# Performance work log

Measured on AMD Instinct MI355X. Metric: run time of the kernel, lower is better.

## Reference

```python
import jax, jax.numpy as jnp
import numpy as np

BN_INV = 1.0 / np.sqrt(1.0 + 1e-5)  # eval-mode BatchNorm1d with running_mean=0, running_var=1


def _lin_bn_relu(x, W, g, b):
    # Linear(no bias) -> BN(eval) -> ReLU
    return jax.nn.relu((x @ W.T) * (g * BN_INV) + b)


def setup_inputs() -> dict:
    key = jax.random.key(0)
    ks = jax.random.split(key, 24)
    B, P, N, C, H, OUT = 8, 1024, 20, 32, 256, 256
    s = 0.05
    inp = {
        "polylines": jax.random.normal(ks[0], (B, P, N, C), dtype=jnp.float32),
        "polylines_mask": jax.random.randint(ks[1], (B, P, N), 0, 2) > 0,
        # pre_mlps: [Lin(C->H,no bias)+BN+ReLU] x2, Lin(H->H, bias)
        "pre_w0": jax.random.normal(ks[2], (H, C), dtype=jnp.float32) * s,
        "pre_g0": jnp.ones((H,), jnp.float32),
        "pre_b0": jnp.zeros((H,), jnp.float32),
        "pre_w1": jax.random.normal(ks[3], (H, H), dtype=jnp.float32) * s,
        "pre_g1": jnp.ones((H,), jnp.float32),
        "pre_b1": jnp.zeros((H,), jnp.float32),
        "pre_w2": jax.random.normal(ks[4], (H, H), dtype=jnp.float32) * s,
        "pre_bias2": jnp.zeros((H,), jnp.float32),
        # mlps: c_in=2H -> [H,H,H]
        "mlp_w0": jax.random.normal(ks[5], (H, 2 * H), dtype=jnp.float32) * s,
        "mlp_g0": jnp.ones((H,), jnp.float32),
        "mlp_b0": jnp.zeros((H,), jnp.float32),
        "mlp_w1": jax.random.normal(ks[6], (H, H), dtype=jnp.float32) * s,
        "mlp_g1": jnp.ones((H,), jnp.float32),
        "mlp_b1": jnp.zeros((H,), jnp.float32),
        "mlp_w2": jax.random.normal(ks[7], (H, H), dtype=jnp.float32) * s,
        "mlp_bias2": jnp.zeros((H,), jnp.float32),
        # out_mlps (without_norm): Lin(H->H,bias)+ReLU, Lin(H->OUT,bias)
        "out_w0": jax.random.normal(ks[8], (H, H), dtype=jnp.float32) * s,
        "out_b0": jnp.zeros((H,), jnp.float32),
        "out_w1": jax.random.normal(ks[9], (OUT, H), dtype=jnp.float32) * s,
        "out_b1": jnp.zeros((OUT,), jnp.float32),
    }
    return inp


def reference(polylines, polylines_mask,
              pre_w0, pre_g0, pre_b0, pre_w1, pre_g1, pre_b1, pre_w2, pre_bias2,
              mlp_w0, mlp_g0, mlp_b0, mlp_w1, mlp_g1, mlp_b1, mlp_w2, mlp_bias2,
              out_w0, out_b0, out_w1, out_b1):
    # gather->MLP->zero-scatter is equivalent to dense MLP followed by mask-zeroing
    # (all per-point ops are elementwise / last-dim matmuls).
    m = polylines_mask[..., None].astype(polylines.dtype)  # (B,P,N,1)

    x = _lin_bn_relu(polylines, pre_w0, pre_g0, pre_b0)
    x = _lin_bn_relu(x, pre_w1, pre_g1, pre_b1)
    x = (x @ pre_w2.T + pre_bias2) * m                      # (B,P,N,H) zero at invalid

    pooled = x.max(axis=2)                                  # (B,P,H) max over zero-filled buffer
    x = jnp.concatenate(
        [x, jnp.broadcast_to(pooled[:, :, None, :], x.shape)], axis=-1)  # (B,P,N,2H)

    x = _lin_bn_relu(x, mlp_w0, mlp_g0, mlp_b0)
    x = _lin_bn_relu(x, mlp_w1, mlp_g1, mlp_b1)
    x = (x @ mlp_w2.T + mlp_bias2) * m                      # (B,P,N,H)

    buf = x.max(axis=2)                                     # (B,P,H)

    valid = jnp.any(polylines_mask, axis=-1)                # sum(mask)>0
    y = jax.nn.relu(buf @ out_w0.T + out_b0)
    y = (y @ out_w1.T + out_b1) * valid[..., None].astype(buf.dtype)  # (B,P,OUT)
    return y
```

## Files before the change

kernel.cpp:

```cpp
#include <hip/hip_runtime.h>
#include <stdint.h>
#include <stddef.h>

typedef __bf16 bf16;
typedef __bf16 bf16x4 __attribute__((ext_vector_type(4)));
typedef __bf16 bf16x8 __attribute__((ext_vector_type(8)));
typedef float f32x4 __attribute__((ext_vector_type(4)));
typedef float f32x16 __attribute__((ext_vector_type(16)));

#define BNI 0.9999950000374996f
#define NROW 240
#define NPOLYB 12
#define TOTROW 163840
#define NPOLY 8192
#define NBLK 683

#define AADDR(r, ch) ((r)*256 + ((((ch) ^ ((r)&31)))<<3))

#define OFF_ACT  0
#define OFF_WB0  122880
#define OFF_WB1  139264
#define OFF_T2   155648
#define OFF_VAL  161792
#define LDS_TOTAL 161840

#define WS_PRE_W0 0
#define WS_PRE_W1 8192
#define WS_PRE_W2 73728
#define WS_MLP_W0 139264
#define WS_MLP_W1 270336
#define WS_MLP_W2 335872
#define WS_OUT_W0 401408
#define WS_OUT_W1 466944

__device__ __forceinline__ bf16 f2b(float f){
  unsigned int i = __builtin_bit_cast(unsigned int, f);
  unsigned int r = i + 0x7fffu + ((i >> 16) & 1u);
  unsigned short h = (unsigned short)(r >> 16);
  return __builtin_bit_cast(bf16, h);
}
__device__ __forceinline__ float b2f(bf16 x){
  unsigned short u = __builtin_bit_cast(unsigned short, x);
  union { unsigned int i; float f; } v; v.i = ((unsigned int)u) << 16; return v.f;
}
__device__ __forceinline__ bf16x8 ld8f(const float* p, float sc){
  f32x4 a = *(const f32x4*)p;
  f32x4 b = *(const f32x4*)(p + 4);
  bf16x8 r;
  #pragma unroll
  for (int j = 0; j < 4; ++j){ r[j] = f2b(a[j]*sc); r[4+j] = f2b(b[j]*sc); }
  return r;
}

__global__ __launch_bounds__(256)
void prep_kernel(const float* s0, const float* s1, const float* s2, const float* s3,
                 const float* s4, const float* s5, const float* s6, const float* s7,
                 const float* g0, const float* g1, const float* g3, const float* g4,
                 bf16* dst)
{
  const int offs[8] = {WS_PRE_W0, WS_PRE_W1, WS_PRE_W2, WS_MLP_W0,
                       WS_MLP_W1, WS_MLP_W2, WS_OUT_W0, WS_OUT_W1};
  const int sz[8]   = {8192, 65536, 65536, 131072, 65536, 65536, 65536, 65536};
  const int ld[8]   = {32, 256, 256, 512, 256, 256, 256, 256};
  int r = blockIdx.y;
  const float* src = s0;
  if (r == 1) src = s1; else if (r == 2) src = s2; else if (r == 3) src = s3;
  else if (r == 4) src = s4; else if (r == 5) src = s5; else if (r == 6) src = s6;
  else if (r == 7) src = s7;
  const float* gp = (r==0)?g0:(r==1)?g1:(r==3)?g3:(r==4)?g4:nullptr;
  int i = (blockIdx.x*256 + threadIdx.x)*8;
  if (i < sz[r]){
    float sc = gp ? gp[i/ld[r]]*BNI : 1.0f;
    *(bf16x8*)&dst[offs[r] + i] = ld8f(src + i, sc);
  }
}

__device__ __forceinline__ void stageAsync32(const bf16* W, int ldK, int nt, bf16* buf, int tid){
  int wv = tid >> 6;
  #pragma unroll
  for (int i = 0; i < 2; ++i){
    int id = tid + 512*i;
    int fr = id >> 5, kcd = id & 31;
    int kcs = kcd ^ (fr & 31);
    const bf16* g = W + (size_t)(nt*32 + fr)*ldK + kcs*8;
    bf16* l = buf + (size_t)(wv*64 + 512*i)*8;
    __builtin_amdgcn_global_load_lds(
        (const __attribute__((address_space(1))) void*)g,
        (__attribute__((address_space(3))) void*)l,
        16, 0, 0);
  }
}

template<int RELU, int MASK, int ADDT2>
__device__ __forceinline__ void epiT(
    const f32x16& acc, int nt, int row, int poly, float mk, bool valid,
    bf16* sAct, const bf16* sT2, const float* bptr, int hi)
{
  #pragma unroll
  for (int q2 = 0; q2 < 4; ++q2){
    int f0 = nt*32 + 8*q2 + 4*hi;
    f32x4 bb = *(const f32x4*)(bptr + f0);
    bf16x4 tv = {};
    if (ADDT2) tv = *(const bf16x4*)&sT2[poly*256 + f0];
    bf16x4 o;
    #pragma unroll
    for (int j = 0; j < 4; ++j){
      float v = acc[4*q2 + j];
      if (ADDT2) v += b2f(tv[j]);
      v += bb[j];
      if (RELU) v = fmaxf(v, 0.0f);
      if (MASK) v *= mk;
      o[j] = f2b(v);
    }
    if (valid)
      *(bf16x4*)&sAct[row*256 + (((nt*4 + q2) ^ (row & 31))<<3) + 4*hi] = o;
  }
}

template<int RELU, int MASK, int ADDT2>
__device__ __forceinline__ void layerT(
    bf16* sAct, bf16* wb0, bf16* wb1, const bf16* sT2,
    const bf16* W, int ldK, const float* bptr,
    const int* maskp, int blk, int row, int rowc, int lane32, int hi, int tid)
{
  bf16x8 B[16];
  #pragma unroll
  for (int t = 0; t < 16; ++t)
    B[t] = *(const bf16x8*)&sAct[AADDR(rowc, 2*t + hi)];

  float mk = 1.0f;
  if (MASK){
    int g = blk*NROW + row;
    mk = (row < NROW && g < TOTROW && maskp[g]) ? 1.0f : 0.0f;
  }
  const int poly = rowc/20;
  const bool valid = row < NROW;

  stageAsync32(W, ldK, 0, wb0, tid);
  __syncthreads();
  #pragma unroll 1
  for (int c = 0; c < 8; ++c){
    const bf16* cur = (c & 1) ? wb1 : wb0;
    bf16* nxt = (c & 1) ? wb0 : wb1;
    if (c < 7) stageAsync32(W, ldK, c + 1, nxt, tid);
    bf16x8 wf[16];
    const bf16* base = cur + lane32*256;
    #pragma unroll
    for (int t = 0; t < 16; ++t)
      wf[t] = *(const bf16x8*)(base + (((2*t + hi) ^ (lane32 & 31))<<3));
    f32x16 acc = {};
    #pragma unroll
    for (int t = 0; t < 16; ++t)
      acc = __builtin_amdgcn_mfma_f32_32x32x16_bf16(wf[t], B[t], acc, 0, 0, 0);
    epiT<RELU,MASK,ADDT2>(acc, c, row, poly, mk, valid, sAct, sT2, bptr, hi);
    __syncthreads();
  }
}

__device__ __forceinline__ void poolT(const bf16* sAct, bf16* sPool, int tid){
  if (tid < 384){
    int poly = tid >> 5, c = tid & 31;
    float m[8];
    bf16x8 v0 = *(const bf16x8*)&sAct[AADDR(poly*20, c)];
    #pragma unroll
    for (int j = 0; j < 8; ++j) m[j] = b2f(v0[j]);
    for (int r = 1; r < 20; ++r){
      bf16x8 v = *(const bf16x8*)&sAct[AADDR(poly*20 + r, c)];
      #pragma unroll
      for (int j = 0; j < 8; ++j) m[j] = fmaxf(m[j], b2f(v[j]));
    }
    bf16x8 o;
    #pragma unroll
    for (int j = 0; j < 8; ++j) o[j] = f2b(m[j]);
    *(bf16x8*)&sPool[AADDR(poly, c)] = o;
  }
}

__global__ __launch_bounds__(512) __attribute__((amdgpu_waves_per_eu(2, 2)))
void traj_kernel(const float* __restrict__ poly, const int* __restrict__ maskp,
                 const float* pre_b0, const float* pre_b1, const float* pre_bias2,
                 const float* mlp_b0, const float* mlp_b1, const float* mlp_bias2,
                 const float* out_b0, const float* out_b1,
                 const bf16* __restrict__ ws,
                 float* __restrict__ outp)
{
  extern __shared__ char smem[];
  bf16*  sAct   = (bf16*)(smem + OFF_ACT);
  bf16*  wb0    = (bf16*)(smem + OFF_WB0);
  bf16*  wb1    = (bf16*)(smem + OFF_WB1);
  bf16*  sT2    = (bf16*)(smem + OFF_T2);
  float* sValid = (float*)(smem + OFF_VAL);
  bf16*  sPool  = wb0;
  bf16*  sY     = sAct;

  const int tid = threadIdx.x;
  const int w = tid >> 6, L = tid & 63, lane32 = L & 31, hi = L >> 5;
  const int row  = w*32 + lane32;
  const int rowc = row < NROW ? row : NROW - 1;
  const int blk = blockIdx.x;

  const bf16* pw0 = ws + WS_PRE_W0;
  const bf16* pw1 = ws + WS_PRE_W1;
  const bf16* pw2 = ws + WS_PRE_W2;
  const bf16* mw0 = ws + WS_MLP_W0;
  const bf16* mw1 = ws + WS_MLP_W1;
  const bf16* mw2 = ws + WS_MLP_W2;
  const bf16* ow0 = ws + WS_OUT_W0;
  const bf16* ow1 = ws + WS_OUT_W1;

  #pragma unroll
  for (int i = 0; i < 2; ++i){
    int id = tid + 512*i;
    if (id < 960){
      int r = id >> 2, c = id & 3;
      int grow = blk*NROW + r;
      bf16x8 v = {};
      if (grow < TOTROW) v = ld8f(poly + (size_t)grow*32 + c*8, 1.0f);
      *(bf16x8*)&sAct[AADDR(r, c)] = v;
    }
  }
  __syncthreads();
  if (tid < NPOLYB){
    float v = 0.0f;
    #pragma unroll
    for (int r = 0; r < 20; ++r){
      int g = blk*NROW + tid*20 + r;
      if (g < TOTROW && maskp[g]) v = 1.0f;
    }
    sValid[tid] = v;
  }

  {
    bf16x8 B0 = *(const bf16x8*)&sAct[AADDR(rowc, hi)];
    bf16x8 B1 = *(const bf16x8*)&sAct[AADDR(rowc, 2 + hi)];
    #pragma unroll 1
    for (int nt = 0; nt < 8; ++nt){
      const bf16* p = pw0 + (size_t)(nt*32 + lane32)*32 + 8*hi;
      bf16x8 w0 = *(const bf16x8*)p;
      bf16x8 w1 = *(const bf16x8*)(p + 16);
      f32x16 acc = {};
      acc = __builtin_amdgcn_mfma_f32_32x32x16_bf16(w0, B0, acc, 0, 0, 0);
      acc = __builtin_amdgcn_mfma_f32_32x32x16_bf16(w1, B1, acc, 0, 0, 0);
      epiT<1,0,0>(acc, nt, row, 0, 1.0f, row < NROW, sAct, sT2, pre_b0, hi);
    }
  }
  __syncthreads();

  layerT<1,0,0>(sAct, wb0, wb1, sT2, pw1, 256, pre_b1,    maskp, blk, row, rowc, lane32, hi, tid);
  layerT<0,1,0>(sAct, wb0, wb1, sT2, pw2, 256, pre_bias2, maskp, blk, row, rowc, lane32, hi, tid);

  poolT(sAct, sPool, tid);
  __syncthreads();

  {
    bf16x8 Bp[16];
    #pragma unroll
    for (int t = 0; t < 16; ++t)
      Bp[t] = *(const bf16x8*)&sPool[AADDR((lane32 < NPOLYB ? lane32 : 0), 2*t + hi)];
    int nt = w;
    const bf16* p = mw0 + (size_t)(nt*32 + lane32)*512 + 256 + 8*hi;
    f32x16 acc = {};
    #pragma unroll
    for (int t = 0; t < 16; ++t){
      bf16x8 wf = *(const bf16x8*)(p + 16*t);
      acc = __builtin_amdgcn_mfma_f32_32x32x16_bf16(wf, Bp[t], acc, 0, 0, 0);
    }
    if (lane32 < NPOLYB){
      #pragma unroll
      for (int q2 = 0; q2 < 4; ++q2){
        int f0 = nt*32 + 8*q2 + 4*hi;
        bf16x4 o;
        #pragma unroll
        for (int j = 0; j < 4; ++j) o[j] = f2b(acc[4*q2 + j]);
        *(bf16x4*)&sT2[lane32*256 + f0] = o;
      }
    }
  }
  __syncthreads();

  layerT<1,0,1>(sAct, wb0, wb1, sT2, mw0, 512, mlp_b0,    maskp, blk, row, rowc, lane32, hi, tid);
  layerT<1,0,0>(sAct, wb0, wb1, sT2, mw1, 256, mlp_b1,    maskp, blk, row, rowc, lane32, hi, tid);
  layerT<0,1,0>(sAct, wb0, wb1, sT2, mw2, 256, mlp_bias2, maskp, blk, row, rowc, lane32, hi, tid);

  poolT(sAct, sPool, tid);
  __syncthreads();

  {
    bf16x8 Bp[16];
    #pragma unroll
    for (int t = 0; t < 16; ++t)
      Bp[t] = *(const bf16x8*)&sPool[AADDR((lane32 < NPOLYB ? lane32 : 0), 2*t + hi)];
    int nt = w;
    const bf16* p = ow0 + (size_t)(nt*32 + lane32)*256 + 8*hi;
    f32x16 acc = {};
    #pragma unroll
    for (int t = 0; t < 16; ++t){
      bf16x8 wf = *(const bf16x8*)(p + 16*t);
      acc = __builtin_amdgcn_mfma_f32_32x32x16_bf16(wf, Bp[t], acc, 0, 0, 0);
    }
    if (lane32 < NPOLYB){
      #pragma unroll
      for (int q2 = 0; q2 < 4; ++q2){
        int f0 = nt*32 + 8*q2 + 4*hi;
        f32x4 bb = *(const f32x4*)(out_b0 + f0);
        bf16x4 o;
        #pragma unroll
        for (int j = 0; j < 4; ++j) o[j] = f2b(fmaxf(acc[4*q2 + j] + bb[j], 0.0f));
        *(bf16x4*)&sY[lane32*256 + (((nt*4 + q2) ^ (lane32 & 31))<<3) + 4*hi] = o;
      }
    }
  }
  __syncthreads();

  {
    bf16x8 By[16];
    #pragma unroll
    for (int t = 0; t < 16; ++t)
      By[t] = *(const bf16x8*)&sY[AADDR((lane32 < NPOLYB ? lane32 : 0), 2*t + hi)];
    int gp = blk*NPOLYB + lane32;
    float vd = (lane32 < NPOLYB) ? sValid[lane32] : 0.0f;
    int nt = w;
    const bf16* p = ow1 + (size_t)(nt*32 + lane32)*256 + 8*hi;
    f32x16 acc = {};
    #pragma unroll
    for (int t = 0; t < 16; ++t){
      bf16x8 wf = *(const bf16x8*)(p + 16*t);
      acc = __builtin_amdgcn_mfma_f32_32x32x16_bf16(wf, By[t], acc, 0, 0, 0);
    }
    if (lane32 < NPOLYB && gp < NPOLY){
      #pragma unroll
      for (int q2 = 0; q2 < 4; ++q2){
        int f0 = nt*32 + 8*q2 + 4*hi;
        f32x4 bb = *(const f32x4*)(out_b1 + f0);
        f32x4 o;
        #pragma unroll
        for (int j = 0; j < 4; ++j) o[j] = (acc[4*q2 + j] + bb[j]) * vd;
        *(f32x4*)&outp[(size_t)gp*256 + f0] = o;
      }
    }
  }
}

extern "C" void kernel_launch(void* const* d_in, const int* in_sizes, int n_in,
                              void* d_out, int out_size, void* d_ws, size_t ws_size,
                              hipStream_t stream)
{
  const float* poly      = (const float*)d_in[0];
  const int*   maskp     = (const int*)  d_in[1];
  const float* pre_w0    = (const float*)d_in[2];
  const float* pre_g0    = (const float*)d_in[3];
  const float* pre_b0    = (const float*)d_in[4];
  const float* pre_w1    = (const float*)d_in[5];
  const float* pre_g1    = (const float*)d_in[6];
  const float* pre_b1    = (const float*)d_in[7];
  const float* pre_w2    = (const float*)d_in[8];
  const float* pre_bias2 = (const float*)d_in[9];
  const float* mlp_w0    = (const float*)d_in[10];
  const float* mlp_g0    = (const float*)d_in[11];
  const float* mlp_b0    = (const float*)d_in[12];
  const float* mlp_w1    = (const float*)d_in[13];
  const float* mlp_g1    = (const float*)d_in[14];
  const float* mlp_b1    = (const float*)d_in[15];
  const float* mlp_w2    = (const float*)d_in[16];
  const float* mlp_bias2 = (const float*)d_in[17];
  const float* out_w0    = (const float*)d_in[18];
  const float* out_b0    = (const float*)d_in[19];
  const float* out_w1    = (const float*)d_in[20];
  const float* out_b1    = (const float*)d_in[21];

  bf16* ws = (bf16*)d_ws;

  (void)hipFuncSetAttribute((const void*)&traj_kernel,
                            hipFuncAttributeMaxDynamicSharedMemorySize, LDS_TOTAL);

  prep_kernel<<<dim3(64, 8), dim3(256), 0, stream>>>(
      pre_w0, pre_w1, pre_w2, mlp_w0, mlp_w1, mlp_w2, out_w0, out_w1,
      pre_g0, pre_g1, mlp_g0, mlp_g1, ws);

  traj_kernel<<<dim3(NBLK), dim3(512), LDS_TOTAL, stream>>>(
      poly, maskp,
      pre_b0, pre_b1, pre_bias2,
      mlp_b0, mlp_b1, mlp_bias2,
      out_b0, out_b1,
      ws, (float*)d_out);
}
```

Baseline: 303.9 us.

## Double block to 1024 threads, splitting output tiles across two wave groups

Measured after the change: 326.0 us. +7.3%, slower.

```diff
diff --git a/kernel.cpp b/kernel.cpp
--- a/kernel.cpp
+++ b/kernel.cpp
@@ -19,7 +19,6 @@
 
 #define OFF_ACT  0
 #define OFF_WB0  122880
-#define OFF_WB1  139264
 #define OFF_T2   155648
 #define OFF_VAL  161792
 #define LDS_TOTAL 161840
@@ -75,20 +74,17 @@
   }
 }
 
-__device__ __forceinline__ void stageAsync32(const bf16* W, int ldK, int nt, bf16* buf, int tid){
-  int wv = tid >> 6;
-  #pragma unroll
-  for (int i = 0; i < 2; ++i){
-    int id = tid + 512*i;
-    int fr = id >> 5, kcd = id & 31;
-    int kcs = kcd ^ (fr & 31);
-    const bf16* g = W + (size_t)(nt*32 + fr)*ldK + kcs*8;
-    bf16* l = buf + (size_t)(wv*64 + 512*i)*8;
-    __builtin_amdgcn_global_load_lds(
-        (const __attribute__((address_space(1))) void*)g,
-        (__attribute__((address_space(3))) void*)l,
-        16, 0, 0);
-  }
+__device__ __forceinline__ void stageAsyncG(const bf16* W, int ldK, int tile, int kh,
+                                            bf16* buf, int wg, int lane){
+  int id = wg*64 + lane;
+  int fr = id >> 4, kcd = id & 15;
+  int kcs = kcd ^ (fr & 15);
+  const bf16* gp = W + (size_t)(tile*32 + fr)*ldK + kh*128 + kcs*8;
+  bf16* l = buf + (size_t)(wg*64)*8;
+  __builtin_amdgcn_global_load_lds(
+      (const __attribute__((address_space(1))) void*)gp,
+      (__attribute__((address_space(3))) void*)l,
+      16, 0, 0);
 }
 
 template<int RELU, int MASK, int ADDT2>
@@ -118,10 +114,11 @@
 }
 
 template<int RELU, int MASK, int ADDT2>
-__device__ __forceinline__ void layerT(
-    bf16* sAct, bf16* wb0, bf16* wb1, const bf16* sT2,
+__device__ __forceinline__ void layerT16(
+    bf16* sAct, bf16* wbase, const bf16* sT2,
     const bf16* W, int ldK, const float* bptr,
-    const int* maskp, int blk, int row, int rowc, int lane32, int hi, int tid)
+    const int* maskp, int blk, int g, int wg, int row, int rowc,
+    int lane32, int hi, int lane)
 {
   bf16x8 B[16];
   #pragma unroll
@@ -130,29 +127,45 @@
 
   float mk = 1.0f;
   if (MASK){
-    int g = blk*NROW + row;
-    mk = (row < NROW && g < TOTROW && maskp[g]) ? 1.0f : 0.0f;
+    int gr = blk*NROW + row;
+    mk = (row < NROW && gr < TOTROW && maskp[gr]) ? 1.0f : 0.0f;
   }
   const int poly = rowc/20;
   const bool valid = row < NROW;
-
-  stageAsync32(W, ldK, 0, wb0, tid);
+  bf16* bufA = wbase + (size_t)(2*g)*4096;
+  bf16* bufB = bufA + 4096;
+
+  stageAsyncG(W, ldK, g*4, 0, bufA, wg, lane);
   __syncthreads();
   #pragma unroll 1
-  for (int c = 0; c < 8; ++c){
-    const bf16* cur = (c & 1) ? wb1 : wb0;
-    bf16* nxt = (c & 1) ? wb0 : wb1;
-    if (c < 7) stageAsync32(W, ldK, c + 1, nxt, tid);
-    bf16x8 wf[16];
-    const bf16* base = cur + lane32*256;
-    #pragma unroll
-    for (int t = 0; t < 16; ++t)
-      wf[t] = *(const bf16x8*)(base + (((2*t + hi) ^ (lane32 & 31))<<3));
-    f32x16 acc = {};
-    #pragma unroll
-    for (int t = 0; t < 16; ++t)
-      acc = __builtin_amdgcn_mfma_f32_32x32x16_bf16(wf[t], B[t], acc, 0, 0, 0);
-    epiT<RELU,MASK,ADDT2>(acc, c, row, poly, mk, valid, sAct, sT2, bptr, hi);
+  for (int p = 0; p < 4; ++p){
+    f32x16 acc;
+    stageAsyncG(W, ldK, g*4 + p, 1, bufB, wg, lane);
+    {
+      bf16x8 wf[8];
+      const bf16* base = bufA + lane32*128;
+      #pragma unroll
+      for (int t = 0; t < 8; ++t)
+        wf[t] = *(const bf16x8*)(base + (((2*t + hi) ^ (lane32 & 15))<<3));
+      #pragma unroll
+      for (int j = 0; j < 16; ++j) acc[j] = 0.0f;
+      #pragma unroll
+      for (int t = 0; t < 8; ++t)
+        acc = __builtin_amdgcn_mfma_f32_32x32x16_bf16(wf[t], B[t], acc, 0, 0, 0);
+    }
+    __syncthreads();
+    if (p < 3) stageAsyncG(W, ldK, g*4 + p + 1, 0, bufA, wg, lane);
+    {
+      bf16x8 wf[8];
+      const bf16* base = bufB + lane32*128;
+      #pragma unroll
+      for (int t = 0; t < 8; ++t)
+        wf[t] = *(const bf16x8*)(base + (((2*t + hi) ^ (lane32 & 15))<<3));
+      #pragma unroll
+      for (int t = 0; t < 8; ++t)
+        acc = __builtin_amdgcn_mfma_f32_32x32x16_bf16(wf[t], B[8 + t], acc, 0, 0, 0);
+      epiT<RELU,MASK,ADDT2>(acc, g*4 + p, row, poly, mk, valid, sAct, sT2, bptr, hi);
+    }
     __syncthreads();
   }
 }
@@ -176,7 +189,7 @@
   }
 }
 
-__global__ __launch_bounds__(512) __attribute__((amdgpu_waves_per_eu(2, 2)))
+__global__ __launch_bounds__(1024) __attribute__((amdgpu_waves_per_eu(4, 4)))
 void traj_kernel(const float* __restrict__ poly, const int* __restrict__ maskp,
                  const float* pre_b0, const float* pre_b1, const float* pre_bias2,
                  const float* mlp_b0, const float* mlp_b1, const float* mlp_bias2,
@@ -186,16 +199,16 @@
 {
   extern __shared__ char smem[];
   bf16*  sAct   = (bf16*)(smem + OFF_ACT);
-  bf16*  wb0    = (bf16*)(smem + OFF_WB0);
-  bf16*  wb1    = (bf16*)(smem + OFF_WB1);
+  bf16*  wbase  = (bf16*)(smem + OFF_WB0);
   bf16*  sT2    = (bf16*)(smem + OFF_T2);
   float* sValid = (float*)(smem + OFF_VAL);
-  bf16*  sPool  = wb0;
+  bf16*  sPool  = wbase;
   bf16*  sY     = sAct;
 
   const int tid = threadIdx.x;
   const int w = tid >> 6, L = tid & 63, lane32 = L & 31, hi = L >> 5;
-  const int row  = w*32 + lane32;
+  const int g = w >> 3, wg = w & 7;
+  const int row  = wg*32 + lane32;
   const int rowc = row < NROW ? row : NROW - 1;
   const int blk = blockIdx.x;
 
@@ -208,24 +221,20 @@
   const bf16* ow0 = ws + WS_OUT_W0;
   const bf16* ow1 = ws + WS_OUT_W1;
 
-  #pragma unroll
-  for (int i = 0; i < 2; ++i){
-    int id = tid + 512*i;
-    if (id < 960){
-      int r = id >> 2, c = id & 3;
-      int grow = blk*NROW + r;
-      bf16x8 v = {};
-      if (grow < TOTROW) v = ld8f(poly + (size_t)grow*32 + c*8, 1.0f);
-      *(bf16x8*)&sAct[AADDR(r, c)] = v;
-    }
+  if (tid < 960){
+    int r = tid >> 2, c = tid & 3;
+    int grow = blk*NROW + r;
+    bf16x8 v = {};
+    if (grow < TOTROW) v = ld8f(poly + (size_t)grow*32 + c*8, 1.0f);
+    *(bf16x8*)&sAct[AADDR(r, c)] = v;
   }
   __syncthreads();
   if (tid < NPOLYB){
     float v = 0.0f;
     #pragma unroll
     for (int r = 0; r < 20; ++r){
-      int g = blk*NROW + tid*20 + r;
-      if (g < TOTROW && maskp[g]) v = 1.0f;
+      int gg = blk*NROW + tid*20 + r;
+      if (gg < TOTROW && maskp[gg]) v = 1.0f;
     }
     sValid[tid] = v;
   }
@@ -233,8 +242,10 @@
   {
     bf16x8 B0 = *(const bf16x8*)&sAct[AADDR(rowc, hi)];
     bf16x8 B1 = *(const bf16x8*)&sAct[AADDR(rowc, 2 + hi)];
+    __syncthreads();
     #pragma unroll 1
-    for (int nt = 0; nt < 8; ++nt){
+    for (int ntl = 0; ntl < 4; ++ntl){
+      int nt = g*4 + ntl;
       const bf16* p = pw0 + (size_t)(nt*32 + lane32)*32 + 8*hi;
       bf16x8 w0 = *(const bf16x8*)p;
       bf16x8 w1 = *(const bf16x8*)(p + 16);
@@ -246,13 +257,13 @@
   }
   __syncthreads();
 
-  layerT<1,0,0>(sAct, wb0, wb1, sT2, pw1, 256, pre_b1,    maskp, blk, row, rowc, lane32, hi, tid);
-  layerT<0,1,0>(sAct, wb0, wb1, sT2, pw2, 256, pre_bias2, maskp, blk, row, rowc, lane32, hi, tid);
+  layerT16<1,0,0>(sAct, wbase, sT2, pw1, 256, pre_b1,    maskp, blk, g, wg, row, rowc, lane32, hi, L);
+  layerT16<0,1,0>(sAct, wbase, sT2, pw2, 256, pre_bias2, maskp, blk, g, wg, row, rowc, lane32, hi, L);
 
   poolT(sAct, sPool, tid);
   __syncthreads();
 
-  {
+  if (w < 8){
     bf16x8 Bp[16];
     #pragma unroll
     for (int t = 0; t < 16; ++t)
@@ -278,14 +289,14 @@
   }
   __syncthreads();
 
-  layerT<1,0,1>(sAct, wb0, wb1, sT2, mw0, 512, mlp_b0,    maskp, blk, row, rowc, lane32, hi, tid);
-  layerT<1,0,0>(sAct, wb0, wb1, sT2, mw1, 256, mlp_b1,    maskp, blk, row, rowc, lane32, hi, tid);
-  layerT<0,1,0>(sAct, wb0, wb1, sT2, mw2, 256, mlp_bias2, maskp, blk, row, rowc, lane32, hi, tid);
+  layerT16<1,0,1>(sAct, wbase, sT2, mw0, 512, mlp_b0,    maskp, blk, g, wg, row, rowc, lane32, hi, L);
+  layerT16<1,0,0>(sAct, wbase, sT2, mw1, 256, mlp_b1,    maskp, blk, g, wg, row, rowc, lane32, hi, L);
+  layerT16<0,1,0>(sAct, wbase, sT2, mw2, 256, mlp_bias2, maskp, blk, g, wg, row, rowc, lane32, hi, L);
 
   poolT(sAct, sPool, tid);
   __syncthreads();
 
-  {
+  if (w < 8){
     bf16x8 Bp[16];
     #pragma unroll
     for (int t = 0; t < 16; ++t)
@@ -312,7 +323,7 @@
   }
   __syncthreads();
 
-  {
+  if (w < 8){
     bf16x8 By[16];
     #pragma unroll
     for (int t = 0; t < 16; ++t)
@@ -377,7 +388,7 @@
       pre_w0, pre_w1, pre_w2, mlp_w0, mlp_w1, mlp_w2, out_w0, out_w1,
       pre_g0, pre_g1, mlp_g0, mlp_g1, ws);
 
-  traj_kernel<<<dim3(NBLK), dim3(512), LDS_TOTAL, stream>>>(
+  traj_kernel<<<dim3(NBLK), dim3(1024), LDS_TOTAL, stream>>>(
       poly, maskp,
       pre_b0, pre_b1, pre_bias2,
       mlp_b0, mlp_b1, mlp_bias2,
```

## Halve block to 4 waves, each wave computing two row tiles per weight fragment

Applied to the files above, without the earlier changes.

After: 371.1 us. 1.22x slower.

```diff
diff --git a/kernel.cpp b/kernel.cpp
--- a/kernel.cpp
+++ b/kernel.cpp
@@ -78,12 +78,12 @@
 __device__ __forceinline__ void stageAsync32(const bf16* W, int ldK, int nt, bf16* buf, int tid){
   int wv = tid >> 6;
   #pragma unroll
-  for (int i = 0; i < 2; ++i){
-    int id = tid + 512*i;
+  for (int i = 0; i < 4; ++i){
+    int id = tid + 256*i;
     int fr = id >> 5, kcd = id & 31;
     int kcs = kcd ^ (fr & 31);
     const bf16* g = W + (size_t)(nt*32 + fr)*ldK + kcs*8;
-    bf16* l = buf + (size_t)(wv*64 + 512*i)*8;
+    bf16* l = buf + (size_t)(wv*64 + 256*i)*8;
     __builtin_amdgcn_global_load_lds(
         (const __attribute__((address_space(1))) void*)g,
         (__attribute__((address_space(3))) void*)l,
@@ -118,23 +118,53 @@
 }
 
 template<int RELU, int MASK, int ADDT2>
-__device__ __forceinline__ void layerT(
+__device__ __forceinline__ void epiTb(
+    const f32x16& acc, int nt, int row, int poly, float mk, bool valid,
+    bf16* sAct, const bf16* sT2, int hi,
+    const f32x4& bbA, const f32x4& bbB, const f32x4& bbC, const f32x4& bbD)
+{
+  #pragma unroll
+  for (int q2 = 0; q2 < 4; ++q2){
+    int f0 = nt*32 + 8*q2 + 4*hi;
+    f32x4 bb = (q2==0) ? bbA : (q2==1) ? bbB : (q2==2) ? bbC : bbD;
+    bf16x4 tv = {};
+    if (ADDT2) tv = *(const bf16x4*)&sT2[poly*256 + f0];
+    bf16x4 o;
+    #pragma unroll
+    for (int j = 0; j < 4; ++j){
+      float v = acc[4*q2 + j];
+      if (ADDT2) v += b2f(tv[j]);
+      v += bb[j];
+      if (RELU) v = fmaxf(v, 0.0f);
+      if (MASK) v *= mk;
+      o[j] = f2b(v);
+    }
+    if (valid)
+      *(bf16x4*)&sAct[row*256 + (((nt*4 + q2) ^ (row & 31))<<3) + 4*hi] = o;
+  }
+}
+
+template<int RELU, int MASK, int ADDT2>
+__device__ __forceinline__ void layerW4(
     bf16* sAct, bf16* wb0, bf16* wb1, const bf16* sT2,
     const bf16* W, int ldK, const float* bptr,
-    const int* maskp, int blk, int row, int rowc, int lane32, int hi, int tid)
-{
-  bf16x8 B[16];
-  #pragma unroll
-  for (int t = 0; t < 16; ++t)
-    B[t] = *(const bf16x8*)&sAct[AADDR(rowc, 2*t + hi)];
-
-  float mk = 1.0f;
+    const int* maskp, int blk, int row0, int row1,
+    int rowc0, int rowc1, int lane32, int hi, int tid)
+{
+  bf16x8 B0[16], B1[16];
+  #pragma unroll
+  for (int t = 0; t < 16; ++t){
+    B0[t] = *(const bf16x8*)&sAct[AADDR(rowc0, 2*t + hi)];
+    B1[t] = *(const bf16x8*)&sAct[AADDR(rowc1, 2*t + hi)];
+  }
+  float mk0 = 1.0f, mk1 = 1.0f;
   if (MASK){
-    int g = blk*NROW + row;
-    mk = (row < NROW && g < TOTROW && maskp[g]) ? 1.0f : 0.0f;
-  }
-  const int poly = rowc/20;
-  const bool valid = row < NROW;
+    int g0 = blk*NROW + row0, g1 = blk*NROW + row1;
+    mk0 = (row0 < NROW && g0 < TOTROW && maskp[g0]) ? 1.0f : 0.0f;
+    mk1 = (row1 < NROW && g1 < TOTROW && maskp[g1]) ? 1.0f : 0.0f;
+  }
+  const int poly0 = rowc0/20, poly1 = rowc1/20;
+  const bool valid0 = row0 < NROW, valid1 = row1 < NROW;
 
   stageAsync32(W, ldK, 0, wb0, tid);
   __syncthreads();
@@ -143,23 +173,28 @@
     const bf16* cur = (c & 1) ? wb1 : wb0;
     bf16* nxt = (c & 1) ? wb0 : wb1;
     if (c < 7) stageAsync32(W, ldK, c + 1, nxt, tid);
-    bf16x8 wf[16];
+    const float* bp = bptr + c*32 + 4*hi;
+    f32x4 bbA = *(const f32x4*)(bp);
+    f32x4 bbB = *(const f32x4*)(bp + 8);
+    f32x4 bbC = *(const f32x4*)(bp + 16);
+    f32x4 bbD = *(const f32x4*)(bp + 24);
+    f32x16 acc0 = {}, acc1 = {};
     const bf16* base = cur + lane32*256;
     #pragma unroll
-    for (int t = 0; t < 16; ++t)
-      wf[t] = *(const bf16x8*)(base + (((2*t + hi) ^ (lane32 & 31))<<3));
-    f32x16 acc = {};
-    #pragma unroll
-    for (int t = 0; t < 16; ++t)
-      acc = __builtin_amdgcn_mfma_f32_32x32x16_bf16(wf[t], B[t], acc, 0, 0, 0);
-    epiT<RELU,MASK,ADDT2>(acc, c, row, poly, mk, valid, sAct, sT2, bptr, hi);
+    for (int t = 0; t < 16; ++t){
+      bf16x8 wf = *(const bf16x8*)(base + (((2*t + hi) ^ (lane32 & 31))<<3));
+      acc0 = __builtin_amdgcn_mfma_f32_32x32x16_bf16(wf, B0[t], acc0, 0, 0, 0);
+      acc1 = __builtin_amdgcn_mfma_f32_32x32x16_bf16(wf, B1[t], acc1, 0, 0, 0);
+    }
+    epiTb<RELU,MASK,ADDT2>(acc0, c, row0, poly0, mk0, valid0, sAct, sT2, hi, bbA, bbB, bbC, bbD);
+    epiTb<RELU,MASK,ADDT2>(acc1, c, row1, poly1, mk1, valid1, sAct, sT2, hi, bbA, bbB, bbC, bbD);
     __syncthreads();
   }
 }
 
 __device__ __forceinline__ void poolT(const bf16* sAct, bf16* sPool, int tid){
-  if (tid < 384){
-    int poly = tid >> 5, c = tid & 31;
+  for (int u = tid; u < 384; u += 256){
+    int poly = u >> 5, c = u & 31;
     float m[8];
     bf16x8 v0 = *(const bf16x8*)&sAct[AADDR(poly*20, c)];
     #pragma unroll
@@ -176,7 +211,7 @@
   }
 }
 
-__global__ __launch_bounds__(512) __attribute__((amdgpu_waves_per_eu(2, 2)))
+__global__ __launch_bounds__(256) __attribute__((amdgpu_waves_per_eu(1, 1)))
 void traj_kernel(const float* __restrict__ poly, const int* __restrict__ maskp,
                  const float* pre_b0, const float* pre_b1, const float* pre_bias2,
                  const float* mlp_b0, const float* mlp_b1, const float* mlp_bias2,
@@ -195,8 +230,10 @@
 
   const int tid = threadIdx.x;
   const int w = tid >> 6, L = tid & 63, lane32 = L & 31, hi = L >> 5;
-  const int row  = w*32 + lane32;
-  const int rowc = row < NROW ? row : NROW - 1;
+  const int row0 = w*64 + lane32;
+  const int row1 = row0 + 32;
+  const int rowc0 = row0 < NROW ? row0 : NROW - 1;
+  const int rowc1 = row1 < NROW ? row1 : NROW - 1;
   const int blk = blockIdx.x;
 
   const bf16* pw0 = ws + WS_PRE_W0;
@@ -209,8 +246,8 @@
   const bf16* ow1 = ws + WS_OUT_W1;
 
   #pragma unroll
-  for (int i = 0; i < 2; ++i){
-    int id = tid + 512*i;
+  for (int i = 0; i < 4; ++i){
+    int id = tid + 256*i;
     if (id < 960){
       int r = id >> 2, c = id & 3;
       int grow = blk*NROW + r;
@@ -231,23 +268,28 @@
   }
 
   {
-    bf16x8 B0 = *(const bf16x8*)&sAct[AADDR(rowc, hi)];
-    bf16x8 B1 = *(const bf16x8*)&sAct[AADDR(rowc, 2 + hi)];
+    bf16x8 B00 = *(const bf16x8*)&sAct[AADDR(rowc0, hi)];
+    bf16x8 B01 = *(const bf16x8*)&sAct[AADDR(rowc0, 2 + hi)];
+    bf16x8 B10 = *(const bf16x8*)&sAct[AADDR(rowc1, hi)];
+    bf16x8 B11 = *(const bf16x8*)&sAct[AADDR(rowc1, 2 + hi)];
     #pragma unroll 1
     for (int nt = 0; nt < 8; ++nt){
       const bf16* p = pw0 + (size_t)(nt*32 + lane32)*32 + 8*hi;
       bf16x8 w0 = *(const bf16x8*)p;
       bf16x8 w1 = *(const bf16x8*)(p + 16);
-      f32x16 acc = {};
-      acc = __builtin_amdgcn_mfma_f32_32x32x16_bf16(w0, B0, acc, 0, 0, 0);
-      acc = __builtin_amdgcn_mfma_f32_32x32x16_bf16(w1, B1, acc, 0, 0, 0);
-      epiT<1,0,0>(acc, nt, row, 0, 1.0f, row < NROW, sAct, sT2, pre_b0, hi);
-    }
-  }
-  __syncthreads();
-
-  layerT<1,0,0>(sAct, wb0, wb1, sT2, pw1, 256, pre_b1,    maskp, blk, row, rowc, lane32, hi, tid);
-  layerT<0,1,0>(sAct, wb0, wb1, sT2, pw2, 256, pre_bias2, maskp, blk, row, rowc, lane32, hi, tid);
+      f32x16 acc0 = {}, acc1 = {};
+      acc0 = __builtin_amdgcn_mfma_f32_32x32x16_bf16(w0, B00, acc0, 0, 0, 0);
+      acc0 = __builtin_amdgcn_mfma_f32_32x32x16_bf16(w1, B01, acc0, 0, 0, 0);
+      acc1 = __builtin_amdgcn_mfma_f32_32x32x16_bf16(w0, B10, acc1, 0, 0, 0);
+      acc1 = __builtin_amdgcn_mfma_f32_32x32x16_bf16(w1, B11, acc1, 0, 0, 0);
+      epiT<1,0,0>(acc0, nt, row0, 0, 1.0f, row0 < NROW, sAct, sT2, pre_b0, hi);
+      epiT<1,0,0>(acc1, nt, row1, 0, 1.0f, row1 < NROW, sAct, sT2, pre_b0, hi);
+    }
+  }
+  __syncthreads();
+
+  layerW4<1,0,0>(sAct, wb0, wb1, sT2, pw1, 256, pre_b1,    maskp, blk, row0, row1, rowc0, rowc1, lane32, hi, tid);
+  layerW4<0,1,0>(sAct, wb0, wb1, sT2, pw2, 256, pre_bias2, maskp, blk, row0, row1, rowc0, rowc1, lane32, hi, tid);
 
   poolT(sAct, sPool, tid);
   __syncthreads();
@@ -257,30 +299,33 @@
     #pragma unroll
     for (int t = 0; t < 16; ++t)
       Bp[t] = *(const bf16x8*)&sPool[AADDR((lane32 < NPOLYB ? lane32 : 0), 2*t + hi)];
-    int nt = w;
-    const bf16* p = mw0 + (size_t)(nt*32 + lane32)*512 + 256 + 8*hi;
-    f32x16 acc = {};
-    #pragma unroll
-    for (int t = 0; t < 16; ++t){
-      bf16x8 wf = *(const bf16x8*)(p + 16*t);
-      acc = __builtin_amdgcn_mfma_f32_32x32x16_bf16(wf, Bp[t], acc, 0, 0, 0);
-    }
-    if (lane32 < NPOLYB){
+    #pragma unroll 1
+    for (int it = 0; it < 2; ++it){
+      int nt = w + 4*it;
+      const bf16* p = mw0 + (size_t)(nt*32 + lane32)*512 + 256 + 8*hi;
+      f32x16 acc = {};
       #pragma unroll
-      for (int q2 = 0; q2 < 4; ++q2){
-        int f0 = nt*32 + 8*q2 + 4*hi;
-        bf16x4 o;
+      for (int t = 0; t < 16; ++t){
+        bf16x8 wf = *(const bf16x8*)(p + 16*t);
+        acc = __builtin_amdgcn_mfma_f32_32x32x16_bf16(wf, Bp[t], acc, 0, 0, 0);
+      }
+      if (lane32 < NPOLYB){
         #pragma unroll
-        for (int j = 0; j < 4; ++j) o[j] = f2b(acc[4*q2 + j]);
-        *(bf16x4*)&sT2[lane32*256 + f0] = o;
-      }
-    }
-  }
-  __syncthreads();
-
-  layerT<1,0,1>(sAct, wb0, wb1, sT2, mw0, 512, mlp_b0,    maskp, blk, row, rowc, lane32, hi, tid);
-  layerT<1,0,0>(sAct, wb0, wb1, sT2, mw1, 256, mlp_b1,    maskp, blk, row, rowc, lane32, hi, tid);
-  layerT<0,1,0>(sAct, wb0, wb1, sT2, mw2, 256, mlp_bias2, maskp, blk, row, rowc, lane32, hi, tid);
+        for (int q2 = 0; q2 < 4; ++q2){
+          int f0 = nt*32 + 8*q2 + 4*hi;
+          bf16x4 o;
+          #pragma unroll
+          for (int j = 0; j < 4; ++j) o[j] = f2b(acc[4*q2 + j]);
+          *(bf16x4*)&sT2[lane32*256 + f0] = o;
+        }
+      }
+    }
+  }
+  __syncthreads();
+
+  layerW4<1,0,1>(sAct, wb0, wb1, sT2, mw0, 512, mlp_b0,    maskp, blk, row0, row1, rowc0, rowc1, lane32, hi, tid);
+  layerW4<1,0,0>(sAct, wb0, wb1, sT2, mw1, 256, mlp_b1,    maskp, blk, row0, row1, rowc0, rowc1, lane32, hi, tid);
+  layerW4<0,1,0>(sAct, wb0, wb1, sT2, mw2, 256, mlp_bias2, maskp, blk, row0, row1, rowc0, rowc1, lane32, hi, tid);
 
   poolT(sAct, sPool, tid);
   __syncthreads();
@@ -290,23 +335,26 @@
     #pragma unroll
     for (int t = 0; t < 16; ++t)
       Bp[t] = *(const bf16x8*)&sPool[AADDR((lane32 < NPOLYB ? lane32 : 0), 2*t + hi)];
-    int nt = w;
-    const bf16* p = ow0 + (size_t)(nt*32 + lane32)*256 + 8*hi;
-    f32x16 acc = {};
-    #pragma unroll
-    for (int t = 0; t < 16; ++t){
-      bf16x8 wf = *(const bf16x8*)(p + 16*t);
-      acc = __builtin_amdgcn_mfma_f32_32x32x16_bf16(wf, Bp[t], acc, 0, 0, 0);
-    }
-    if (lane32 < NPOLYB){
+    #pragma unroll 1
+    for (int it = 0; it < 2; ++it){
+      int nt = w + 4*it;
+      const bf16* p = ow0 + (size_t)(nt*32 + lane32)*256 + 8*hi;
+      f32x16 acc = {};
       #pragma unroll
-      for (int q2 = 0; q2 < 4; ++q2){
-        int f0 = nt*32 + 8*q2 + 4*hi;
-        f32x4 bb = *(const f32x4*)(out_b0 + f0);
-        bf16x4 o;
+      for (int t = 0; t < 16; ++t){
+        bf16x8 wf = *(const bf16x8*)(p + 16*t);
+        acc = __builtin_amdgcn_mfma_f32_32x32x16_bf16(wf, Bp[t], acc, 0, 0, 0);
+      }
+      if (lane32 < NPOLYB){
         #pragma unroll
-        for (int j = 0; j < 4; ++j) o[j] = f2b(fmaxf(acc[4*q2 + j] + bb[j], 0.0f));
-        *(bf16x4*)&sY[lane32*256 + (((nt*4 + q2) ^ (lane32 & 31))<<3) + 4*hi] = o;
+        for (int q2 = 0; q2 < 4; ++q2){
+          int f0 = nt*32 + 8*q2 + 4*hi;
+          f32x4 bb = *(const f32x4*)(out_b0 + f0);
+          bf16x4 o;
+          #pragma unroll
+          for (int j = 0; j < 4; ++j) o[j] = f2b(fmaxf(acc[4*q2 + j] + bb[j], 0.0f));
+          *(bf16x4*)&sY[lane32*256 + (((nt*4 + q2) ^ (lane32 & 31))<<3) + 4*hi] = o;
+        }
       }
     }
   }
@@ -319,23 +367,26 @@
       By[t] = *(const bf16x8*)&sY[AADDR((lane32 < NPOLYB ? lane32 : 0), 2*t + hi)];
     int gp = blk*NPOLYB + lane32;
     float vd = (lane32 < NPOLYB) ? sValid[lane32] : 0.0f;
-    int nt = w;
-    const bf16* p = ow1 + (size_t)(nt*32 + lane32)*256 + 8*hi;
-    f32x16 acc = {};
-    #pragma unroll
-    for (int t = 0; t < 16; ++t){
-      bf16x8 wf = *(const bf16x8*)(p + 16*t);
-      acc = __builtin_amdgcn_mfma_f32_32x32x16_bf16(wf, By[t], acc, 0, 0, 0);
-    }
-    if (lane32 < NPOLYB && gp < NPOLY){
+    #pragma unroll 1
+    for (int it = 0; it < 2; ++it){
+      int nt = w + 4*it;
+      const bf16* p = ow1 + (size_t)(nt*32 + lane32)*256 + 8*hi;
+      f32x16 acc = {};
       #pragma unroll
-      for (int q2 = 0; q2 < 4; ++q2){
-        int f0 = nt*32 + 8*q2 + 4*hi;
-        f32x4 bb = *(const f32x4*)(out_b1 + f0);
-        f32x4 o;
+      for (int t = 0; t < 16; ++t){
+        bf16x8 wf = *(const bf16x8*)(p + 16*t);
+        acc = __builtin_amdgcn_mfma_f32_32x32x16_bf16(wf, By[t], acc, 0, 0, 0);
+      }
+      if (lane32 < NPOLYB && gp < NPOLY){
         #pragma unroll
-        for (int j = 0; j < 4; ++j) o[j] = (acc[4*q2 + j] + bb[j]) * vd;
-        *(f32x4*)&outp[(size_t)gp*256 + f0] = o;
+        for (int q2 = 0; q2 < 4; ++q2){
+          int f0 = nt*32 + 8*q2 + 4*hi;
+          f32x4 bb = *(const f32x4*)(out_b1 + f0);
+          f32x4 o;
+          #pragma unroll
+          for (int j = 0; j < 4; ++j) o[j] = (acc[4*q2 + j] + bb[j]) * vd;
+          *(f32x4*)&outp[(size_t)gp*256 + f0] = o;
+        }
       }
     }
   }
@@ -377,7 +428,7 @@
       pre_w0, pre_w1, pre_w2, mlp_w0, mlp_w1, mlp_w2, out_w0, out_w1,
       pre_g0, pre_g1, mlp_g0, mlp_g1, ws);
 
-  traj_kernel<<<dim3(NBLK), dim3(512), LDS_TOTAL, stream>>>(
+  traj_kernel<<<dim3(NBLK), dim3(256), LDS_TOTAL, stream>>>(
       poly, maskp,
       pre_b0, pre_b1, pre_bias2,
       mlp_b0, mlp_b1, mlp_bias2,
```

## Pre-swizzle weights into MFMA fragment order and read them directly from global

Applied to the files above, without the earlier changes.

Measured after the change: 355.5 us. 17.0% more time.

```diff
diff --git a/kernel.cpp b/kernel.cpp
--- a/kernel.cpp
+++ b/kernel.cpp
@@ -18,16 +18,16 @@
 #define AADDR(r, ch) ((r)*256 + ((((ch) ^ ((r)&31)))<<3))
 
 #define OFF_ACT  0
-#define OFF_WB0  122880
-#define OFF_WB1  139264
-#define OFF_T2   155648
-#define OFF_VAL  161792
-#define LDS_TOTAL 161840
+#define OFF_POOL 122880
+#define OFF_T2   129024
+#define OFF_VAL  135168
+#define LDS_TOTAL 135216
 
 #define WS_PRE_W0 0
 #define WS_PRE_W1 8192
 #define WS_PRE_W2 73728
 #define WS_MLP_W0 139264
+#define WS_MLP_W0T (139264 + 65536)
 #define WS_MLP_W1 270336
 #define WS_MLP_W2 335872
 #define WS_OUT_W0 401408
@@ -68,26 +68,19 @@
   else if (r == 4) src = s4; else if (r == 5) src = s5; else if (r == 6) src = s6;
   else if (r == 7) src = s7;
   const float* gp = (r==0)?g0:(r==1)?g1:(r==3)?g3:(r==4)?g4:nullptr;
-  int i = (blockIdx.x*256 + threadIdx.x)*8;
-  if (i < sz[r]){
-    float sc = gp ? gp[i/ld[r]]*BNI : 1.0f;
-    *(bf16x8*)&dst[offs[r] + i] = ld8f(src + i, sc);
-  }
-}
-
-__device__ __forceinline__ void stageAsync32(const bf16* W, int ldK, int nt, bf16* buf, int tid){
-  int wv = tid >> 6;
-  #pragma unroll
-  for (int i = 0; i < 2; ++i){
-    int id = tid + 512*i;
-    int fr = id >> 5, kcd = id & 31;
-    int kcs = kcd ^ (fr & 31);
-    const bf16* g = W + (size_t)(nt*32 + fr)*ldK + kcs*8;
-    bf16* l = buf + (size_t)(wv*64 + 512*i)*8;
-    __builtin_amdgcn_global_load_lds(
-        (const __attribute__((address_space(1))) void*)g,
-        (__attribute__((address_space(3))) void*)l,
-        16, 0, 0);
+  int gid = blockIdx.x*256 + threadIdx.x;
+  int ldv = ld[r];
+  if (gid < (sz[r] >> 3)){
+    int l, t, nt, colbase = 0;
+    if (ldv == 512){ colbase = (gid >> 13)*256; int g2 = gid & 8191;
+                     l = g2 & 63; t = (g2 >> 6) & 15; nt = g2 >> 10; }
+    else if (ldv == 256){ l = gid & 63; t = (gid >> 6) & 15; nt = gid >> 10; }
+    else { l = gid & 63; t = (gid >> 6) & 1; nt = gid >> 7; }
+    int srow = nt*32 + (l & 31);
+    int scol = colbase + t*16 + (l >> 5)*8;
+    float sc = gp ? gp[srow]*BNI : 1.0f;
+    *(bf16x8*)&dst[offs[r] + (size_t)gid*8] =
+        ld8f(src + (size_t)srow*ldv + scol, sc);
   }
 }
 
@@ -118,10 +111,9 @@
 }
 
 template<int RELU, int MASK, int ADDT2>
-__device__ __forceinline__ void layerT(
-    bf16* sAct, bf16* wb0, bf16* wb1, const bf16* sT2,
-    const bf16* W, int ldK, const float* bptr,
-    const int* maskp, int blk, int row, int rowc, int lane32, int hi, int tid)
+__device__ __forceinline__ void layerG(
+    bf16* sAct, const bf16* sT2, const bf16* __restrict__ Wf, const float* bptr,
+    const int* maskp, int blk, int row, int rowc, int hi, int L)
 {
   bf16x8 B[16];
   #pragma unroll
@@ -136,24 +128,16 @@
   const int poly = rowc/20;
   const bool valid = row < NROW;
 
-  stageAsync32(W, ldK, 0, wb0, tid);
-  __syncthreads();
   #pragma unroll 1
-  for (int c = 0; c < 8; ++c){
-    const bf16* cur = (c & 1) ? wb1 : wb0;
-    bf16* nxt = (c & 1) ? wb0 : wb1;
-    if (c < 7) stageAsync32(W, ldK, c + 1, nxt, tid);
-    bf16x8 wf[16];
-    const bf16* base = cur + lane32*256;
-    #pragma unroll
-    for (int t = 0; t < 16; ++t)
-      wf[t] = *(const bf16x8*)(base + (((2*t + hi) ^ (lane32 & 31))<<3));
+  for (int nt = 0; nt < 8; ++nt){
+    const bf16* p = Wf + (size_t)nt*8192 + (size_t)L*8;
     f32x16 acc = {};
     #pragma unroll
-    for (int t = 0; t < 16; ++t)
-      acc = __builtin_amdgcn_mfma_f32_32x32x16_bf16(wf[t], B[t], acc, 0, 0, 0);
-    epiT<RELU,MASK,ADDT2>(acc, c, row, poly, mk, valid, sAct, sT2, bptr, hi);
-    __syncthreads();
+    for (int t = 0; t < 16; ++t){
+      bf16x8 wf = *(const bf16x8*)(p + t*512);
+      acc = __builtin_amdgcn_mfma_f32_32x32x16_bf16(wf, B[t], acc, 0, 0, 0);
+    }
+    epiT<RELU,MASK,ADDT2>(acc, nt, row, poly, mk, valid, sAct, sT2, bptr, hi);
   }
 }
 
@@ -186,11 +170,9 @@
 {
   extern __shared__ char smem[];
   bf16*  sAct   = (bf16*)(smem + OFF_ACT);
-  bf16*  wb0    = (bf16*)(smem + OFF_WB0);
-  bf16*  wb1    = (bf16*)(smem + OFF_WB1);
+  bf16*  sPool  = (bf16*)(smem + OFF_POOL);
   bf16*  sT2    = (bf16*)(smem + OFF_T2);
   float* sValid = (float*)(smem + OFF_VAL);
-  bf16*  sPool  = wb0;
   bf16*  sY     = sAct;
 
   const int tid = threadIdx.x;
@@ -203,6 +185,7 @@
   const bf16* pw1 = ws + WS_PRE_W1;
   const bf16* pw2 = ws + WS_PRE_W2;
   const bf16* mw0 = ws + WS_MLP_W0;
+  const bf16* mw0t= ws + WS_MLP_W0T;
   const bf16* mw1 = ws + WS_MLP_W1;
   const bf16* mw2 = ws + WS_MLP_W2;
   const bf16* ow0 = ws + WS_OUT_W0;
@@ -235,20 +218,20 @@
     bf16x8 B1 = *(const bf16x8*)&sAct[AADDR(rowc, 2 + hi)];
     #pragma unroll 1
     for (int nt = 0; nt < 8; ++nt){
-      const bf16* p = pw0 + (size_t)(nt*32 + lane32)*32 + 8*hi;
+      const bf16* p = pw0 + (size_t)nt*1024 + (size_t)L*8;
       bf16x8 w0 = *(const bf16x8*)p;
-      bf16x8 w1 = *(const bf16x8*)(p + 16);
+      bf16x8 w1 = *(const bf16x8*)(p + 512);
       f32x16 acc = {};
       acc = __builtin_amdgcn_mfma_f32_32x32x16_bf16(w0, B0, acc, 0, 0, 0);
       acc = __builtin_amdgcn_mfma_f32_32x32x16_bf16(w1, B1, acc, 0, 0, 0);
       epiT<1,0,0>(acc, nt, row, 0, 1.0f, row < NROW, sAct, sT2, pre_b0, hi);
     }
   }
-  __syncthreads();
-
-  layerT<1,0,0>(sAct, wb0, wb1, sT2, pw1, 256, pre_b1,    maskp, blk, row, rowc, lane32, hi, tid);
-  layerT<0,1,0>(sAct, wb0, wb1, sT2, pw2, 256, pre_bias2, maskp, blk, row, rowc, lane32, hi, tid);
-
+
+  layerG<1,0,0>(sAct, sT2, pw1, pre_b1,    maskp, blk, row, rowc, hi, L);
+  layerG<0,1,0>(sAct, sT2, pw2, pre_bias2, maskp, blk, row, rowc, hi, L);
+
+  __syncthreads();
   poolT(sAct, sPool, tid);
   __syncthreads();
 
@@ -258,11 +241,11 @@
     for (int t = 0; t < 16; ++t)
       Bp[t] = *(const bf16x8*)&sPool[AADDR((lane32 < NPOLYB ? lane32 : 0), 2*t + hi)];
     int nt = w;
-    const bf16* p = mw0 + (size_t)(nt*32 + lane32)*512 + 256 + 8*hi;
+    const bf16* p = mw0t + (size_t)nt*8192 + (size_t)L*8;
     f32x16 acc = {};
     #pragma unroll
     for (int t = 0; t < 16; ++t){
-      bf16x8 wf = *(const bf16x8*)(p + 16*t);
+      bf16x8 wf = *(const bf16x8*)(p + t*512);
       acc = __builtin_amdgcn_mfma_f32_32x32x16_bf16(wf, Bp[t], acc, 0, 0, 0);
     }
     if (lane32 < NPOLYB){
@@ -278,10 +261,11 @@
   }
   __syncthreads();
 
-  layerT<1,0,1>(sAct, wb0, wb1, sT2, mw0, 512, mlp_b0,    maskp, blk, row, rowc, lane32, hi, tid);
-  layerT<1,0,0>(sAct, wb0, wb1, sT2, mw1, 256, mlp_b1,    maskp, blk, row, rowc, lane32, hi, tid);
-  layerT<0,1,0>(sAct, wb0, wb1, sT2, mw2, 256, mlp_bias2, maskp, blk, row, rowc, lane32, hi, tid);
-
+  layerG<1,0,1>(sAct, sT2, mw0, mlp_b0,    maskp, blk, row, rowc, hi, L);
+  layerG<1,0,0>(sAct, sT2, mw1, mlp_b1,    maskp, blk, row, rowc, hi, L);
+  layerG<0,1,0>(sAct, sT2, mw2, mlp_bias2, maskp, blk, row, rowc, hi, L);
+
+  __syncthreads();
   poolT(sAct, sPool, tid);
   __syncthreads();
 
@@ -291,11 +275,11 @@
     for (int t = 0; t < 16; ++t)
       Bp[t] = *(const bf16x8*)&sPool[AADDR((lane32 < NPOLYB ? lane32 : 0), 2*t + hi)];
     int nt = w;
-    const bf16* p = ow0 + (size_t)(nt*32 + lane32)*256 + 8*hi;
+    const bf16* p = ow0 + (size_t)nt*8192 + (size_t)L*8;
     f32x16 acc = {};
     #pragma unroll
     for (int t = 0; t < 16; ++t){
-      bf16x8 wf = *(const bf16x8*)(p + 16*t);
+      bf16x8 wf = *(const bf16x8*)(p + t*512);
       acc = __builtin_amdgcn_mfma_f32_32x32x16_bf16(wf, Bp[t], acc, 0, 0, 0);
     }
     if (lane32 < NPOLYB){
@@ -320,11 +304,11 @@
     int gp = blk*NPOLYB + lane32;
     float vd = (lane32 < NPOLYB) ? sValid[lane32] : 0.0f;
     int nt = w;
-    const bf16* p = ow1 + (size_t)(nt*32 + lane32)*256 + 8*hi;
+    const bf16* p = ow1 + (size_t)nt*8192 + (size_t)L*8;
     f32x16 acc = {};
     #pragma unroll
     for (int t = 0; t < 16; ++t){
-      bf16x8 wf = *(const bf16x8*)(p + 16*t);
+      bf16x8 wf = *(const bf16x8*)(p + t*512);
       acc = __builtin_amdgcn_mfma_f32_32x32x16_bf16(wf, By[t], acc, 0, 0, 0);
     }
     if (lane32 < NPOLYB && gp < NPOLY){
```
